# Performance work log

Hardware: AMD Instinct MI355X
Metric: run time of the kernel (lower is better)

Reference implementation:

```python
import jax, jax.numpy as jnp
import numpy as np

B, N, D, P = 512, 64, 256, 512   # graphs, nodes/graph, feat dim, pairs/graph
DEG = 16
E = B * N * DEG                  # 524288 edges
H = 512                          # classifier hidden dim
LR_OUT, CR_OUT, MR_OUT = 4, 6, 17


def setup_inputs() -> dict:
    key = jax.random.key(0)
    ks = jax.random.split(key, 20)
    x = jax.random.normal(ks[0], (B * N, D), jnp.float32)
    # edges stay within each graph, as in a collated batch of graphs
    offs_e = jnp.repeat(jnp.arange(B, dtype=jnp.int32) * N, N * DEG)
    src = jax.random.randint(ks[1], (E,), 0, N, dtype=jnp.int32) + offs_e
    dst = jax.random.randint(ks[2], (E,), 0, N, dtype=jnp.int32) + offs_e
    edge_index = jnp.stack([src, dst])
    pairs = jax.random.randint(ks[3], (B, P, 2), 0, N, dtype=jnp.int32)
    s = 0.02
    inp = {
        'x': x, 'edge_index': edge_index, 'pairs': pairs,
        'gcn_w1': jax.random.normal(ks[4], (D, D), jnp.float32) * s,
        'gcn_b1': jnp.zeros((D,), jnp.float32),
        'gcn_w2': jax.random.normal(ks[5], (D, D), jnp.float32) * s,
        'gcn_b2': jnp.zeros((D,), jnp.float32),
        'lr_w1': jax.random.normal(ks[6], (D, H), jnp.float32) * s,
        'lr_b1': jnp.zeros((H,), jnp.float32),
        'lr_w2': jax.random.normal(ks[7], (H, LR_OUT), jnp.float32) * s,
        'lr_b2': jnp.zeros((LR_OUT,), jnp.float32),
        'cr_w1': jax.random.normal(ks[8], (D, H), jnp.float32) * s,
        'cr_b1': jnp.zeros((H,), jnp.float32),
        'cr_w2': jax.random.normal(ks[9], (H, CR_OUT), jnp.float32) * s,
        'cr_b2': jnp.zeros((CR_OUT,), jnp.float32),
        'mr_w1': jax.random.normal(ks[10], (D, H), jnp.float32) * s,
        'mr_b1': jnp.zeros((H,), jnp.float32),
        'mr_w2': jax.random.normal(ks[11], (H, MR_OUT), jnp.float32) * s,
        'mr_b2': jnp.zeros((MR_OUT,), jnp.float32),
    }
    return inp


def _gcn(x, src, dst, gcn_w1, gcn_b1, gcn_w2, gcn_b2):
    # vanilla GCN with self-loops and symmetric normalization
    n_tot = x.shape[0]
    loops = jnp.arange(n_tot, dtype=src.dtype)
    s = jnp.concatenate([src, loops])
    d = jnp.concatenate([dst, loops])
    deg = jax.ops.segment_sum(jnp.ones_like(s, dtype=x.dtype), d, num_segments=n_tot)
    norm = jax.lax.rsqrt(deg[s] * deg[d])  # [E + n_tot]

    def layer(h, W, b, act):
        m = jax.ops.segment_sum(h[s] * norm[:, None], d, num_segments=n_tot)
        o = m @ W + b
        return jax.nn.relu(o) if act else o

    h = layer(x, gcn_w1, gcn_b1, True)
    return layer(h, gcn_w2, gcn_b2, False)


def _mlp(z, w1, b1, w2, b2):
    return jax.nn.relu(z @ w1 + b1) @ w2 + b2


def reference(x, edge_index, pairs,
              gcn_w1, gcn_b1, gcn_w2, gcn_b2,
              lr_w1, lr_b1, lr_w2, lr_b2,
              cr_w1, cr_b1, cr_w2, cr_b2,
              mr_w1, mr_b1, mr_w2, mr_b2):
    emb = _gcn(x, edge_index[0], edge_index[1], gcn_w1, gcn_b1, gcn_w2, gcn_b2)  # [B*N, D]
    # decollate + batched pair gather (replaces the python double loop)
    offs = (jnp.arange(B, dtype=pairs.dtype) * N)[:, None, None]  # [B,1,1]
    gp = pairs + offs                                            # global node ids [B,P,2]
    e0 = emb[gp[..., 0].reshape(-1)].reshape(B, P, D)
    e1 = emb[gp[..., 1].reshape(-1)].reshape(B, P, D)
    ci = 0.5 * (e0 + e1)  # aggregate(emb0, emb1, 'mean')
    lr = _mlp(ci, lr_w1, lr_b1, lr_w2, lr_b2)
    cr = _mlp(ci, cr_w1, cr_b1, cr_w2, cr_b2)
    mr = _mlp(ci, mr_w1, mr_b1, mr_w2, mr_b2)
    return (lr, cr, mr)
```

## Files before the change

kernel.cpp:

```cpp
#include <hip/hip_runtime.h>
#include <hip/hip_bf16.h>

typedef __bf16 bf16x8 __attribute__((ext_vector_type(8)));
typedef __bf16 bf16x4 __attribute__((ext_vector_type(4)));
typedef float f32x16 __attribute__((ext_vector_type(16)));
typedef unsigned short u16x8 __attribute__((ext_vector_type(8)));
typedef unsigned int u32x4 __attribute__((ext_vector_type(4)));

#define E_EDGES 524288
#define OUT_CR_OFF 1048576
#define OUT_MR_OFF 2621440
#define W1TP_ELEMS (48 * 9216)
#define GCNW_ELEMS (2 * 8 * 16 * 64 * 8)
#define WS_NEED ((size_t)(W1TP_ELEMS + GCNW_ELEMS) * 2)

static __device__ __forceinline__ float bf2f_(unsigned short u) {
  unsigned int x = ((unsigned int)u) << 16;
  return __builtin_bit_cast(float, x);
}
static __device__ __forceinline__ unsigned short f2bf_(float f) {
  return __builtin_bit_cast(unsigned short, (__bf16)f);
}
static __device__ __forceinline__ unsigned int pack2_(float a, float b) {
  return ((unsigned int)f2bf_(b) << 16) | (unsigned int)f2bf_(a);
}

__global__ void pack_weights(const float* __restrict__ gw1, const float* __restrict__ gw2,
                             const float* __restrict__ lw1, const float* __restrict__ cw1,
                             const float* __restrict__ mw1,
                             const float* __restrict__ lw2, const float* __restrict__ cw2,
                             const float* __restrict__ mw2,
                             unsigned short* __restrict__ w1tp,
                             unsigned short* __restrict__ gcnw) {
  const int idx = blockIdx.x * 256 + threadIdx.x;
  if (idx < W1TP_ELEMS) {
    const int ht = idx / 9216;
    const int r = idx - ht * 9216;
    const int h = ht >> 4, tt = ht & 15;
    if (r < 8192) {
      const int kc = r >> 8, r2 = r & 255, hidl = r2 >> 3, j = r2 & 7;
      const float* w1 = (h == 0) ? lw1 : (h == 1) ? cw1 : mw1;
      w1tp[idx] = f2bf_(w1[(kc * 8 + j) * 512 + tt * 32 + hidl]);
    } else {
      const int r2 = r - 8192;
      const int q = r2 >> 8, r3 = r2 & 255, o = r3 >> 3, j = r3 & 7;
      const float* w2 = (h == 0) ? lw2 : (h == 1) ? cw2 : mw2;
      const int OUTD = (h == 0) ? 4 : (h == 1) ? 6 : 17;
      w1tp[idx] = (o < OUTD) ? f2bf_(w2[((tt * 4 + q) * 8 + j) * OUTD + o])
                             : (unsigned short)0;
    }
  } else {
    const int g = idx - W1TP_ELEMS;
    if (g < GCNW_ELEMS) {
      const int layer = g >> 16, r = g & 65535;
      const int O = r >> 13, r2 = r & 8191, s = r2 >> 9;
      const int r3 = r2 & 511, lane = r3 >> 3, j = r3 & 7;
      const float* W = layer ? gw2 : gw1;
      gcnw[g] = f2bf_(W[(s * 16 + (lane >> 5) * 8 + j) * 256 + O * 32 + (lane & 31)]);
    }
  }
}

template <bool PACKED>
__launch_bounds__(512, 2)
__global__ void fused_gcn_heads(
    const float* __restrict__ x,
    const int* __restrict__ esrc, const int* __restrict__ edst,
    const int* __restrict__ pairs,
    const float* __restrict__ gw1, const float* __restrict__ gb1,
    const float* __restrict__ gw2, const float* __restrict__ gb2,
    const float* __restrict__ lw1, const float* __restrict__ lb1,
    const float* __restrict__ lw2, const float* __restrict__ lb2,
    const float* __restrict__ cw1, const float* __restrict__ cb1,
    const float* __restrict__ cw2, const float* __restrict__ cb2,
    const float* __restrict__ mw1, const float* __restrict__ mb1,
    const float* __restrict__ mw2, const float* __restrict__ mb2,
    const unsigned short* __restrict__ w1tp,
    const unsigned short* __restrict__ gcnw,
    float* __restrict__ out) {
  __shared__ unsigned short bufM[16384];
  __shared__ union WU {
    struct GG { short eS[1024]; short eD[1024]; short csr[1024]; } g;
    unsigned short wbuf[2][9216];
  } U;
  __shared__ int csroff[65];
  __shared__ float invdeg[64], rdeg[64];
  __shared__ float b1s[1568];

  const int b = blockIdx.x, tid = threadIdx.x;
  const int wv = tid >> 6, lane = tid & 63;
  const int half = lane >> 5, ln = lane & 31;

  auto sidx = [](int node, int boff) {
    return (node * 512 + (boff ^ ((node & 15) << 4))) >> 1;
  };

  {
    const float4* xg = (const float4*)(x + b * 16384);
    for (int i = tid; i < 4096; i += 512) {
      const float4 v = xg[i];
      ushort4 o4;
      o4.x = f2bf_(v.x); o4.y = f2bf_(v.y); o4.z = f2bf_(v.z); o4.w = f2bf_(v.w);
      *(ushort4*)&bufM[sidx(i >> 6, (i & 63) * 8)] = o4;
    }
    const int eb = b * 1024, nb = b * 64;
    for (int i = tid; i < 1024; i += 512) {
      U.g.eS[i] = (short)(esrc[eb + i] - nb);
      U.g.eD[i] = (short)(edst[eb + i] - nb);
    }
  }
  __syncthreads();

  if (tid < 64) {
    const short n = (short)tid;
    int cnt = 0;
    for (int c = 0; c < 128; ++c) {
      const u16x8 dv = *(const u16x8*)&U.g.eD[c * 8];
#pragma unroll
      for (int j = 0; j < 8; ++j) cnt += ((short)dv[j] == n) ? 1 : 0;
    }
    int val = cnt;
#pragma unroll
    for (int off = 1; off < 64; off <<= 1) {
      const int up = __shfl_up(val, off, 64);
      if (tid >= off) val += up;
    }
    csroff[tid] = val - cnt;
    if (tid == 63) csroff[64] = val;
    const float dg = (float)(cnt + 1);
    invdeg[tid] = 1.0f / dg;
    rdeg[tid] = rsqrtf(dg);
    int pos = val - cnt;
    for (int c = 0; c < 128; ++c) {
      const u16x8 dv = *(const u16x8*)&U.g.eD[c * 8];
      const u16x8 sv = *(const u16x8*)&U.g.eS[c * 8];
#pragma unroll
      for (int j = 0; j < 8; ++j)
        if ((short)dv[j] == n) U.g.csr[pos++] = (short)sv[j];
    }
  }
  __syncthreads();

  float4 acc[8];

  auto do_agg = [&]() {
#pragma unroll
    for (int k = 0; k < 8; ++k) {
      const int n = wv * 8 + k;
      const ushort4 xv = *(const ushort4*)&bufM[sidx(n, lane * 8)];
      const float sd = invdeg[n];
      float ax = bf2f_(xv.x) * sd, ay = bf2f_(xv.y) * sd;
      float az = bf2f_(xv.z) * sd, aw = bf2f_(xv.w) * sd;
      const float rn = rdeg[n];
      const int e0 = csroff[n], e1 = csroff[n + 1];
      for (int e = e0; e < e1; ++e) {
        const int s = U.g.csr[e];
        const float wgt = rn * rdeg[s];
        const ushort4 sv = *(const ushort4*)&bufM[sidx(s, lane * 8)];
        ax += bf2f_(sv.x) * wgt; ay += bf2f_(sv.y) * wgt;
        az += bf2f_(sv.z) * wgt; aw += bf2f_(sv.w) * wgt;
      }
      acc[k].x = ax; acc[k].y = ay; acc[k].z = az; acc[k].w = aw;
    }
  };

  auto writeback = [&]() {
#pragma unroll
    for (int k = 0; k < 8; ++k) {
      const int n = wv * 8 + k;
      ushort4 o4;
      o4.x = f2bf_(acc[k].x); o4.y = f2bf_(acc[k].y);
      o4.z = f2bf_(acc[k].z); o4.w = f2bf_(acc[k].w);
      *(ushort4*)&bufM[sidx(n, lane * 8)] = o4;
    }
  };

  auto do_mm = [&](int layer, const float* __restrict__ Wg,
                   const float* __restrict__ bias, bool relu) {
    f32x16 a0, a1;
#pragma unroll
    for (int i = 0; i < 16; ++i) { a0[i] = 0.f; a1[i] = 0.f; }
#pragma unroll
    for (int s = 0; s < 16; ++s) {
      bf16x8 aW;
      if (PACKED) {
        aW = *(const bf16x8*)&gcnw[(((layer * 8 + wv) * 16 + s) * 64 + lane) * 8];
      } else {
#pragma unroll
        for (int j = 0; j < 8; ++j)
          aW[j] = (__bf16)Wg[(s * 16 + half * 8 + j) * 256 + wv * 32 + ln];
      }
      const bf16x8 b0 = *(const bf16x8*)&bufM[sidx(ln, s * 32 + half * 16)];
      const bf16x8 b1v = *(const bf16x8*)&bufM[sidx(32 + ln, s * 32 + half * 16)];
      a0 = __builtin_amdgcn_mfma_f32_32x32x16_bf16(aW, b0, a0, 0, 0, 0);
      a1 = __builtin_amdgcn_mfma_f32_32x32x16_bf16(aW, b1v, a1, 0, 0, 0);
    }
    __syncthreads();
    float4 bb[4];
#pragma unroll
    for (int g4 = 0; g4 < 4; ++g4)
      bb[g4] = *(const float4*)&bias[wv * 32 + g4 * 8 + 4 * half];
#pragma unroll
    for (int N = 0; N < 2; ++N) {
      const int node = N * 32 + ln;
#pragma unroll
      for (int g4 = 0; g4 < 4; ++g4) {
#pragma unroll
        for (int e2 = 0; e2 < 2; ++e2) {
          float v0 = (N ? a1 : a0)[g4 * 4 + e2 * 2 + 0] + bb[g4][e2 * 2 + 0];
          float v1 = (N ? a1 : a0)[g4 * 4 + e2 * 2 + 1] + bb[g4][e2 * 2 + 1];
          if (relu) { v0 = fmaxf(v0, 0.f); v1 = fmaxf(v1, 0.f); }
          const int ocol = wv * 32 + g4 * 8 + 4 * half + e2 * 2;
          *(unsigned int*)&bufM[sidx(node, ocol * 2)] = pack2_(v0, v1);
        }
      }
    }
    __syncthreads();
  };

  do_agg(); __syncthreads(); writeback(); __syncthreads();
  do_mm(0, gw1, gb1, true);
  do_agg(); __syncthreads(); writeback(); __syncthreads();
  do_mm(1, gw2, gb2, false);

  b1s[tid] = lb1[tid];
  b1s[512 + tid] = cb1[tid];
  b1s[1024 + tid] = mb1[tid];
  if (tid < 4) b1s[1536 + tid] = lb2[tid];
  else if (tid < 10) b1s[1536 + tid] = cb2[tid - 4];
  else if (tid < 27) b1s[1536 + tid] = mb2[tid - 10];

  bf16x8 ci[2][16];
#pragma unroll
  for (int pg = 0; pg < 2; ++pg) {
    const int p = wv * 64 + pg * 32 + ln;
    const int2 pr = ((const int2*)pairs)[b * 512 + p];
#pragma unroll
    for (int s = 0; s < 16; ++s) {
      const int boff = s * 32 + half * 16;
      const u16x8 r0 = *(const u16x8*)&bufM[sidx(pr.x, boff)];
      const u16x8 r1 = *(const u16x8*)&bufM[sidx(pr.y, boff)];
      bf16x8 v;
#pragma unroll
      for (int j = 0; j < 8; ++j) v[j] = (__bf16)(0.5f * (bf2f_(r0[j]) + bf2f_(r1[j])));
      ci[pg][s] = v;
    }
  }

  float4 st0, st1, st2;
  float w1r[16]; float w2r[4];
  const int hidl = tid & 31, kc2 = tid >> 5;

  auto stage_issue = [&](int ht) {
    if (PACKED) {
      const float4* g = (const float4*)(w1tp + ht * 9216);
      st0 = g[tid]; st1 = g[tid + 512];
      if (tid < 128) st2 = g[tid + 1024];
    } else {
      const int h = ht >> 4, tt = ht & 15;
      const float* w1p = (h == 0) ? lw1 : (h == 1) ? cw1 : mw1;
      const float* w2p = (h == 0) ? lw2 : (h == 1) ? cw2 : mw2;
      const int OUTD = (h == 0) ? 4 : (h == 1) ? 6 : 17;
#pragma unroll
      for (int r = 0; r < 2; ++r)
#pragma unroll
        for (int j = 0; j < 8; ++j)
          w1r[r * 8 + j] = w1p[((2 * kc2 + r) * 8 + j) * 512 + tt * 32 + hidl];
      if (tid < 256) {
        const int q4 = tid >> 6, rem = tid & 63, o = rem >> 1, jh = rem & 1;
#pragma unroll
        for (int jj = 0; jj < 4; ++jj) {
          const int row = (tt * 4 + q4) * 8 + jh * 4 + jj;
          w2r[jj] = (o < OUTD) ? w2p[row * OUTD + o] : 0.f;
        }
      }
    }
  };
  auto stage_commit = [&](int bi) {
    if (PACKED) {
      float4* d = (float4*)U.wbuf[bi];
      d[tid] = st0; d[tid + 512] = st1;
      if (tid < 128) d[tid + 1024] = st2;
    } else {
#pragma unroll
      for (int r = 0; r < 2; ++r) {
        bf16x8 v;
#pragma unroll
        for (int j = 0; j < 8; ++j) v[j] = (__bf16)w1r[r * 8 + j];
        *(bf16x8*)&U.wbuf[bi][((2 * kc2 + r) * 32 + hidl) * 8] = v;
      }
      if (tid < 256) {
        const int q4 = tid >> 6, rem = tid & 63, o = rem >> 1, jh = rem & 1;
        bf16x4 v4;
#pragma unroll
        for (int jj = 0; jj < 4; ++jj) v4[jj] = (__bf16)w2r[jj];
        *(bf16x4*)&U.wbuf[bi][8192 + (q4 * 32 + o) * 8 + jh * 4] = v4;
      }
    }
  };

  stage_issue(0);
  stage_commit(0);
  __syncthreads();

  f32x16 acc2_0, acc2_1;
  for (int ht = 0; ht < 48; ++ht) {
    const int h = ht >> 4, tt = ht & 15, cur = ht & 1;
    if (tt == 0) {
#pragma unroll
      for (int i = 0; i < 16; ++i) { acc2_0[i] = 0.f; acc2_1[i] = 0.f; }
    }
    if (ht < 47) stage_issue(ht + 1);

    f32x16 p0, p1;
#pragma unroll
    for (int i = 0; i < 16; ++i) { p0[i] = 0.f; p1[i] = 0.f; }
    __builtin_amdgcn_s_setprio(1);
#pragma unroll
    for (int s = 0; s < 16; ++s) {
      const bf16x8 a = *(const bf16x8*)&U.wbuf[cur][((2 * s + half) * 32 + ln) * 8];
      p0 = __builtin_amdgcn_mfma_f32_32x32x16_bf16(a, ci[0][s], p0, 0, 0, 0);
      p1 = __builtin_amdgcn_mfma_f32_32x32x16_bf16(a, ci[1][s], p1, 0, 0, 0);
    }
    __builtin_amdgcn_s_setprio(0);

    const bf16x8 a2k0 = *(const bf16x8*)&U.wbuf[cur][8192 + ((0 + half) * 32 + ln) * 8];
    const bf16x8 a2k1 = *(const bf16x8*)&U.wbuf[cur][8192 + ((2 + half) * 32 + ln) * 8];
    float4 bb[4];
#pragma unroll
    for (int g4 = 0; g4 < 4; ++g4)
      bb[g4] = *(const float4*)&b1s[h * 512 + tt * 32 + g4 * 8 + 4 * half];

#pragma unroll
    for (int pg = 0; pg < 2; ++pg) {
      float hv[16];
#pragma unroll
      for (int i = 0; i < 16; ++i)
        hv[i] = fmaxf((pg ? p1 : p0)[i] + bb[i >> 2][i & 3], 0.f);
#pragma unroll
      for (int ks = 0; ks < 2; ++ks) {
        const int bse = ks * 8;
        const unsigned x0 = pack2_(hv[bse + 0], hv[bse + 1]);
        const unsigned x1 = pack2_(hv[bse + 2], hv[bse + 3]);
        const unsigned y0 = pack2_(hv[bse + 4], hv[bse + 5]);
        const unsigned y1 = pack2_(hv[bse + 6], hv[bse + 7]);
        const unsigned px0 = __shfl_xor(x0, 32);
        const unsigned px1 = __shfl_xor(x1, 32);
        const unsigned py0 = __shfl_xor(y0, 32);
        const unsigned py1 = __shfl_xor(y1, 32);
        u32x4 wt;
        wt[0] = half ? py0 : x0;
        wt[1] = half ? py1 : x1;
        wt[2] = half ? y0 : px0;
        wt[3] = half ? y1 : px1;
        const bf16x8 bfrag = __builtin_bit_cast(bf16x8, wt);
        if (pg == 0)
          acc2_0 = __builtin_amdgcn_mfma_f32_32x32x16_bf16(ks ? a2k1 : a2k0, bfrag,
                                                           acc2_0, 0, 0, 0);
        else
          acc2_1 = __builtin_amdgcn_mfma_f32_32x32x16_bf16(ks ? a2k1 : a2k0, bfrag,
                                                           acc2_1, 0, 0, 0);
      }
    }

    if (ht < 47) stage_commit(cur ^ 1);
    __syncthreads();

    if (tt == 15) {
      const int OUTD = (h == 0) ? 4 : (h == 1) ? 6 : 17;
      float* outp = out + ((h == 0) ? 0 : (h == 1) ? OUT_CR_OFF : OUT_MR_OFF);
      const int b2o = (h == 0) ? 1536 : (h == 1) ? 1540 : 1546;
#pragma unroll
      for (int pg = 0; pg < 2; ++pg) {
        const long qq = (long)b * 512 + wv * 64 + pg * 32 + ln;
#pragma unroll
        for (int g4 = 0; g4 < 4; ++g4) {
#pragma unroll
          for (int e = 0; e < 4; ++e) {
            const int o = g4 * 8 + 4 * half + e;
            if (o < OUTD)
              outp[qq * OUTD + o] = (pg ? acc2_1 : acc2_0)[g4 * 4 + e] + b1s[b2o + o];
          }
        }
      }
    }
  }
}

extern "C" void kernel_launch(void* const* d_in, const int* in_sizes, int n_in,
                              void* d_out, int out_size, void* d_ws, size_t ws_size,
                              hipStream_t stream) {
  (void)in_sizes; (void)n_in; (void)out_size;
  const float* x   = (const float*)d_in[0];
  const int* eidx  = (const int*)d_in[1];
  const int* pairs = (const int*)d_in[2];
  const float* gw1 = (const float*)d_in[3];
  const float* gb1 = (const float*)d_in[4];
  const float* gw2 = (const float*)d_in[5];
  const float* gb2 = (const float*)d_in[6];
  const float* lw1 = (const float*)d_in[7];
  const float* lb1 = (const float*)d_in[8];
  const float* lw2 = (const float*)d_in[9];
  const float* lb2 = (const float*)d_in[10];
  const float* cw1 = (const float*)d_in[11];
  const float* cb1 = (const float*)d_in[12];
  const float* cw2 = (const float*)d_in[13];
  const float* cb2 = (const float*)d_in[14];
  const float* mw1 = (const float*)d_in[15];
  const float* mb1 = (const float*)d_in[16];
  const float* mw2 = (const float*)d_in[17];
  const float* mb2 = (const float*)d_in[18];

  unsigned short* w1tp = (unsigned short*)d_ws;
  unsigned short* gcnw = w1tp + W1TP_ELEMS;

  if (d_ws != nullptr && ws_size >= WS_NEED) {
    pack_weights<<<2240, 256, 0, stream>>>(gw1, gw2, lw1, cw1, mw1, lw2, cw2, mw2,
                                           w1tp, gcnw);
    fused_gcn_heads<true><<<512, 512, 0, stream>>>(
        x, eidx, eidx + E_EDGES, pairs, gw1, gb1, gw2, gb2,
        lw1, lb1, lw2, lb2, cw1, cb1, cw2, cb2, mw1, mb1, mw2, mb2,
        w1tp, gcnw, (float*)d_out);
  } else {
    fused_gcn_heads<false><<<512, 512, 0, stream>>>(
        x, eidx, eidx + E_EDGES, pairs, gw1, gb1, gw2, gb2,
        lw1, lb1, lw2, lb2, cw1, cb1, cw2, cb2, mw1, mb1, mw2, mb2,
        w1tp, gcnw, (float*)d_out);
  }
}
```

Measured before the change: 426.6 us.

## Split classifier into two passes over pairs and unroll edge aggregation by four

The classifier stage now handles 32 pairs per wave per pass, in two passes, instead of 64 pairs at once. This halves the live ci registers and the accumulators, and the pair-dependent MFMA chain is replaced by two independent K-split chains that are summed afterwards. The cost is that all 48 weight tiles are re-staged per pass, which doubles the weight traffic and the barriers. The GCN aggregation loop is also unrolled by four so the LDS gathers for several neighbours can be issued together.

Measured after the change: 430.2 us. About the same (+0.9%).

```diff
diff --git a/kernel.cpp b/kernel.cpp
--- a/kernel.cpp
+++ b/kernel.cpp
@@ -153,7 +153,22 @@
       float az = bf2f_(xv.z) * sd, aw = bf2f_(xv.w) * sd;
       const float rn = rdeg[n];
       const int e0 = csroff[n], e1 = csroff[n + 1];
-      for (int e = e0; e < e1; ++e) {
+      int e = e0;
+      for (; e + 4 <= e1; e += 4) {
+        const int s0 = U.g.csr[e + 0], s1 = U.g.csr[e + 1];
+        const int s2 = U.g.csr[e + 2], s3 = U.g.csr[e + 3];
+        const float w0 = rn * rdeg[s0], w1 = rn * rdeg[s1];
+        const float w2 = rn * rdeg[s2], w3 = rn * rdeg[s3];
+        const ushort4 v0 = *(const ushort4*)&bufM[sidx(s0, lane * 8)];
+        const ushort4 v1 = *(const ushort4*)&bufM[sidx(s1, lane * 8)];
+        const ushort4 v2 = *(const ushort4*)&bufM[sidx(s2, lane * 8)];
+        const ushort4 v3 = *(const ushort4*)&bufM[sidx(s3, lane * 8)];
+        ax += bf2f_(v0.x) * w0 + bf2f_(v1.x) * w1 + bf2f_(v2.x) * w2 + bf2f_(v3.x) * w3;
+        ay += bf2f_(v0.y) * w0 + bf2f_(v1.y) * w1 + bf2f_(v2.y) * w2 + bf2f_(v3.y) * w3;
+        az += bf2f_(v0.z) * w0 + bf2f_(v1.z) * w1 + bf2f_(v2.z) * w2 + bf2f_(v3.z) * w3;
+        aw += bf2f_(v0.w) * w0 + bf2f_(v1.w) * w1 + bf2f_(v2.w) * w2 + bf2f_(v3.w) * w3;
+      }
+      for (; e < e1; ++e) {
         const int s = U.g.csr[e];
         const float wgt = rn * rdeg[s];
         const ushort4 sv = *(const ushort4*)&bufM[sidx(s, lane * 8)];
@@ -229,23 +244,6 @@
   if (tid < 4) b1s[1536 + tid] = lb2[tid];
   else if (tid < 10) b1s[1536 + tid] = cb2[tid - 4];
   else if (tid < 27) b1s[1536 + tid] = mb2[tid - 10];
-
-  bf16x8 ci[2][16];
-#pragma unroll
-  for (int pg = 0; pg < 2; ++pg) {
-    const int p = wv * 64 + pg * 32 + ln;
-    const int2 pr = ((const int2*)pairs)[b * 512 + p];
-#pragma unroll
-    for (int s = 0; s < 16; ++s) {
-      const int boff = s * 32 + half * 16;
-      const u16x8 r0 = *(const u16x8*)&bufM[sidx(pr.x, boff)];
-      const u16x8 r1 = *(const u16x8*)&bufM[sidx(pr.y, boff)];
-      bf16x8 v;
-#pragma unroll
-      for (int j = 0; j < 8; ++j) v[j] = (__bf16)(0.5f * (bf2f_(r0[j]) + bf2f_(r1[j])));
-      ci[pg][s] = v;
-    }
-  }
 
   float4 st0, st1, st2;
   float w1r[16]; float w2r[4];
@@ -299,44 +297,59 @@
     }
   };
 
-  stage_issue(0);
-  stage_commit(0);
-  __syncthreads();
-
-  f32x16 acc2_0, acc2_1;
-  for (int ht = 0; ht < 48; ++ht) {
-    const int h = ht >> 4, tt = ht & 15, cur = ht & 1;
-    if (tt == 0) {
-#pragma unroll
-      for (int i = 0; i < 16; ++i) { acc2_0[i] = 0.f; acc2_1[i] = 0.f; }
-    }
-    if (ht < 47) stage_issue(ht + 1);
-
-    f32x16 p0, p1;
-#pragma unroll
-    for (int i = 0; i < 16; ++i) { p0[i] = 0.f; p1[i] = 0.f; }
-    __builtin_amdgcn_s_setprio(1);
-#pragma unroll
-    for (int s = 0; s < 16; ++s) {
-      const bf16x8 a = *(const bf16x8*)&U.wbuf[cur][((2 * s + half) * 32 + ln) * 8];
-      p0 = __builtin_amdgcn_mfma_f32_32x32x16_bf16(a, ci[0][s], p0, 0, 0, 0);
-      p1 = __builtin_amdgcn_mfma_f32_32x32x16_bf16(a, ci[1][s], p1, 0, 0, 0);
-    }
-    __builtin_amdgcn_s_setprio(0);
-
-    const bf16x8 a2k0 = *(const bf16x8*)&U.wbuf[cur][8192 + ((0 + half) * 32 + ln) * 8];
-    const bf16x8 a2k1 = *(const bf16x8*)&U.wbuf[cur][8192 + ((2 + half) * 32 + ln) * 8];
-    float4 bb[4];
-#pragma unroll
-    for (int g4 = 0; g4 < 4; ++g4)
-      bb[g4] = *(const float4*)&b1s[h * 512 + tt * 32 + g4 * 8 + 4 * half];
-
-#pragma unroll
-    for (int pg = 0; pg < 2; ++pg) {
+  for (int pass = 0; pass < 2; ++pass) {
+    bf16x8 ci[16];
+    {
+      const int p = pass * 256 + wv * 32 + ln;
+      const int2 pr = ((const int2*)pairs)[b * 512 + p];
+#pragma unroll
+      for (int s = 0; s < 16; ++s) {
+        const int boff = s * 32 + half * 16;
+        const u16x8 r0 = *(const u16x8*)&bufM[sidx(pr.x, boff)];
+        const u16x8 r1 = *(const u16x8*)&bufM[sidx(pr.y, boff)];
+        bf16x8 v;
+#pragma unroll
+        for (int j = 0; j < 8; ++j)
+          v[j] = (__bf16)(0.5f * (bf2f_(r0[j]) + bf2f_(r1[j])));
+        ci[s] = v;
+      }
+    }
+
+    stage_issue(0);
+    stage_commit(0);
+    __syncthreads();
+
+    f32x16 acc2;
+    for (int ht = 0; ht < 48; ++ht) {
+      const int h = ht >> 4, tt = ht & 15, cur = ht & 1;
+      if (tt == 0) {
+#pragma unroll
+        for (int i = 0; i < 16; ++i) acc2[i] = 0.f;
+      }
+      if (ht < 47) stage_issue(ht + 1);
+
+      f32x16 pA, pB;
+#pragma unroll
+      for (int i = 0; i < 16; ++i) { pA[i] = 0.f; pB[i] = 0.f; }
+      __builtin_amdgcn_s_setprio(1);
+#pragma unroll
+      for (int s = 0; s < 16; s += 2) {
+        const bf16x8 aE = *(const bf16x8*)&U.wbuf[cur][((2 * s + half) * 32 + ln) * 8];
+        const bf16x8 aO = *(const bf16x8*)&U.wbuf[cur][((2 * s + 2 + half) * 32 + ln) * 8];
+        pA = __builtin_amdgcn_mfma_f32_32x32x16_bf16(aE, ci[s], pA, 0, 0, 0);
+        pB = __builtin_amdgcn_mfma_f32_32x32x16_bf16(aO, ci[s + 1], pB, 0, 0, 0);
+      }
+      __builtin_amdgcn_s_setprio(0);
+
+      const bf16x8 a2k0 = *(const bf16x8*)&U.wbuf[cur][8192 + ((0 + half) * 32 + ln) * 8];
+      const bf16x8 a2k1 = *(const bf16x8*)&U.wbuf[cur][8192 + ((2 + half) * 32 + ln) * 8];
+
       float hv[16];
 #pragma unroll
-      for (int i = 0; i < 16; ++i)
-        hv[i] = fmaxf((pg ? p1 : p0)[i] + bb[i >> 2][i & 3], 0.f);
+      for (int i = 0; i < 16; ++i) {
+        const float bia = b1s[h * 512 + tt * 32 + (i & 3) + 8 * (i >> 2) + 4 * half];
+        hv[i] = fmaxf(pA[i] + pB[i] + bia, 0.f);
+      }
 #pragma unroll
       for (int ks = 0; ks < 2; ++ks) {
         const int bse = ks * 8;
@@ -354,32 +367,24 @@
         wt[2] = half ? y0 : px0;
         wt[3] = half ? y1 : px1;
         const bf16x8 bfrag = __builtin_bit_cast(bf16x8, wt);
-        if (pg == 0)
-          acc2_0 = __builtin_amdgcn_mfma_f32_32x32x16_bf16(ks ? a2k1 : a2k0, bfrag,
-                                                           acc2_0, 0, 0, 0);
-        else
-          acc2_1 = __builtin_amdgcn_mfma_f32_32x32x16_bf16(ks ? a2k1 : a2k0, bfrag,
-                                                           acc2_1, 0, 0, 0);
-      }
-    }
-
-    if (ht < 47) stage_commit(cur ^ 1);
-    __syncthreads();
-
-    if (tt == 15) {
-      const int OUTD = (h == 0) ? 4 : (h == 1) ? 6 : 17;
-      float* outp = out + ((h == 0) ? 0 : (h == 1) ? OUT_CR_OFF : OUT_MR_OFF);
-      const int b2o = (h == 0) ? 1536 : (h == 1) ? 1540 : 1546;
-#pragma unroll
-      for (int pg = 0; pg < 2; ++pg) {
-        const long qq = (long)b * 512 + wv * 64 + pg * 32 + ln;
+        acc2 = __builtin_amdgcn_mfma_f32_32x32x16_bf16(ks ? a2k1 : a2k0, bfrag,
+                                                       acc2, 0, 0, 0);
+      }
+
+      if (ht < 47) stage_commit(cur ^ 1);
+      __syncthreads();
+
+      if (tt == 15) {
+        const int OUTD = (h == 0) ? 4 : (h == 1) ? 6 : 17;
+        float* outp = out + ((h == 0) ? 0 : (h == 1) ? OUT_CR_OFF : OUT_MR_OFF);
+        const int b2o = (h == 0) ? 1536 : (h == 1) ? 1540 : 1546;
+        const long qq = (long)b * 512 + pass * 256 + wv * 32 + ln;
 #pragma unroll
         for (int g4 = 0; g4 < 4; ++g4) {
 #pragma unroll
           for (int e = 0; e < 4; ++e) {
             const int o = g4 * 8 + 4 * half + e;
-            if (o < OUTD)
-              outp[qq * OUTD + o] = (pg ? acc2_1 : acc2_0)[g4 * 4 + e] + b1s[b2o + o];
+            if (o < OUTD) outp[qq * OUTD + o] = acc2[g4 * 4 + e] + b1s[b2o + o];
           }
         }
       }
```
